# Optimization experiments

Measured on AMD Instinct MI355X. Metric: run time of the kernel, lower is better.

Reference implementation:

```python
import jax, jax.numpy as jnp
import numpy as np

# Dimensions
T = 1024      # tokens
D = 1024      # d_model
DFF = 1024    # expert intermediate dim
R = 64        # tucker rank (r_in == r_out)
G = 8         # n_group
E = 32        # experts_per_group
NEXP = G * E  # 256 routed experts
K = 8         # top-k


def setup_inputs() -> dict:
    key = jax.random.key(0)
    ks = jax.random.split(key, 12)
    s = 0.02
    return {
        "x": jax.random.normal(ks[0], (T, D), jnp.float32),
        "Wg": jax.random.normal(ks[1], (D, NEXP), jnp.float32) * s,
        "uin_gate": jax.random.normal(ks[2], (G, D, R), jnp.float32) * s,
        "core_gate": jax.random.normal(ks[3], (G, E, R, R), jnp.float32) * s,
        "uout_gate": jax.random.normal(ks[4], (G, R, DFF), jnp.float32) * s,
        "uin_up": jax.random.normal(ks[5], (G, D, R), jnp.float32) * s,
        "core_up": jax.random.normal(ks[6], (G, E, R, R), jnp.float32) * s,
        "uout_up": jax.random.normal(ks[7], (G, R, DFF), jnp.float32) * s,
        "uin_down": jax.random.normal(ks[8], (G, DFF, R), jnp.float32) * s,
        "core_down": jax.random.normal(ks[9], (G, E, R, R), jnp.float32) * s,
        "uout_down": jax.random.normal(ks[10], (G, R, D), jnp.float32) * s,
    }


def _moe_forward(x, Wg, uin_gate, core_gate, uout_gate,
                 uin_up, core_up, uout_up,
                 uin_down, core_down, uout_down):
    Tn, d = x.shape
    # Router: top-k over 256 experts, softmax over the k logits (fp32 as in torch)
    logits = x @ Wg                                   # [T, NEXP]
    w, sel = jax.lax.top_k(logits, K)                 # [T, K]
    w = jax.nn.softmax(w.astype(jnp.float32), axis=-1).astype(x.dtype)

    e = sel.reshape(-1)                               # [F] global expert id
    g = e // E                                        # [F] group id
    tok = jnp.repeat(jnp.arange(Tn), K)               # [F] source token id
    mask = (g[:, None] == jnp.arange(G)[None, :]).astype(x.dtype)  # [F, G]

    def gather_in(uin):
        # project tokens with every group's u_in once, then gather per pair
        pre = jnp.einsum('td,gdr->gtr', x, uin)       # [G, T, R]
        return pre[g, tok]                            # [F, R]

    def core_apply(xin, core):
        # per-pair Tucker core slice bmm: x.unsqueeze(1) @ core[rel_idx]
        slices = core.reshape(G * E, R, R)[e]         # [F, R, R] gather
        return jnp.einsum('fr,fro->fo', xin, slices)  # [F, R]

    def group_out(h, U):
        # per-pair group-specific projection: h[f] @ U[g_f]
        out = jnp.zeros((h.shape[0], U.shape[-1]), h.dtype)
        for gi in range(G):  # fixed small loop over 8 groups
            out = out + (h * mask[:, gi:gi + 1]) @ U[gi]
        return out

    gate_h = group_out(core_apply(gather_in(uin_gate), core_gate), uout_gate)  # [F, DFF]
    up_h = group_out(core_apply(gather_in(uin_up), core_up), uout_up)          # [F, DFF]
    act = jax.nn.silu(gate_h) * up_h                                           # SwiGLU
    xin_d = group_out(act, uin_down)                                           # [F, R]
    out_f = group_out(core_apply(xin_d, core_down), uout_down)                 # [F, D]
    out_f = out_f * w.reshape(-1)[:, None]
    # scatter-add expert outputs back to tokens
    return jax.ops.segment_sum(out_f, tok, num_segments=Tn)


def reference(x, Wg, uin_gate, core_gate, uout_gate,
              uin_up, core_up, uout_up,
              uin_down, core_down, uout_down):
    return _moe_forward(x, Wg, uin_gate, core_gate, uout_gate,
                        uin_up, core_up, uout_up,
                        uin_down, core_down, uout_down)
```

## Files before the change

### kernel.cpp

```cpp
#include <hip/hip_runtime.h>
#include <hip/hip_bf16.h>
#include <math.h>


#define T_ 1024
#define D_ 1024
#define DFF_ 1024
#define R_ 64
#define G_ 8
#define E_ 32
#define NEXP_ 256
#define K_ 8
#define F_ 8192
#define LKZ_ 8
#define LTB_ 8
#define PKZ_ 2
#define DKZ_ 4
#define LP_ 72

typedef short bf16x8 __attribute__((ext_vector_type(8)));
typedef float f32x4 __attribute__((ext_vector_type(4)));

__device__ __forceinline__ unsigned short f2bf(float f) {
  unsigned int u = __float_as_uint(f);
  u += 0x7fffu + ((u >> 16) & 1u);
  return (unsigned short)(u >> 16);
}

__device__ __forceinline__ void stage_tile(short* dst, const unsigned short* src,
                                           int gp, int tid) {
  for (int idx = tid; idx < 512; idx += 256) {
    int r = idx >> 3, c8 = (idx & 7) << 3;
    *(uint4*)&dst[r * LP_ + c8] = *(const uint4*)&src[(size_t)r * gp + c8];
  }
}

__device__ __forceinline__ void stage_tile_guard(short* dst, const unsigned short* src,
                                                 int gp, int rows_valid, int tid) {
  for (int idx = tid; idx < 512; idx += 256) {
    int r = idx >> 3, c8 = (idx & 7) << 3;
    uint4 v = make_uint4(0u, 0u, 0u, 0u);
    if (r < rows_valid) v = *(const uint4*)&src[(size_t)r * gp + c8];
    *(uint4*)&dst[r * LP_ + c8] = v;
  }
}

__device__ __forceinline__ void mma_strip(const short* As, const short* Bs,
                                          int ms, int lane, f32x4* acc) {
  int lm = lane & 15;
  int lk = (lane >> 4) << 3;
#pragma unroll
  for (int kc = 0; kc < 64; kc += 32) {
    bf16x8 a = *(const bf16x8*)&As[(ms + lm) * LP_ + kc + lk];
#pragma unroll
    for (int nt = 0; nt < 4; ++nt) {
      bf16x8 b = *(const bf16x8*)&Bs[(nt * 16 + lm) * LP_ + kc + lk];
      acc[nt] = __builtin_amdgcn_mfma_f32_16x16x32_bf16(a, b, acc[nt], 0, 0, 0);
    }
  }
}

__global__ __launch_bounds__(256) void k_prep_logits(
    const float* __restrict__ x, const float* __restrict__ Wg,
    const float* __restrict__ s0, const float* __restrict__ s1,
    const float* __restrict__ s2, const float* __restrict__ s3,
    const float* __restrict__ s4, const float* __restrict__ s5,
    unsigned short* __restrict__ xb,
    unsigned short* __restrict__ d0, unsigned short* __restrict__ d1,
    unsigned short* __restrict__ d2, unsigned short* __restrict__ d3,
    unsigned short* __restrict__ d4, unsigned short* __restrict__ d5,
    int* __restrict__ cnt, float* __restrict__ lp) {
  __shared__ float shbuf[64 * 65];
  int b = blockIdx.x;
  if (b < 896) {
    int id = b >> 7, rem = b & 127, g = rem >> 4, tile = rem & 15;
    if (id == 6) {
      size_t base = ((size_t)g * 16 + tile) * 8192;
      for (int i = threadIdx.x; i < 2048; i += 256) {
        size_t idx = base + (size_t)i * 4;
        float4 v = *(const float4*)&x[idx];
        xb[idx + 0] = f2bf(v.x);
        xb[idx + 1] = f2bf(v.y);
        xb[idx + 2] = f2bf(v.z);
        xb[idx + 3] = f2bf(v.w);
      }
      if (g == 0 && tile == 0) cnt[threadIdx.x] = 0;
      return;
    }
    const float* src = id == 0 ? s0 : id == 1 ? s1 : id == 2 ? s2 : id == 3 ? s3 : id == 4 ? s4 : s5;
    unsigned short* dst = id == 0 ? d0 : id == 1 ? d1 : id == 2 ? d2 : id == 3 ? d3 : id == 4 ? d4 : d5;
    if (id < 3) {
      int r0 = tile * 64;
      for (int idx = threadIdx.x; idx < 4096; idx += 256) {
        int r = idx >> 6, c = idx & 63;
        shbuf[r * 65 + c] = src[((size_t)g * 1024 + r0 + r) * 64 + c];
      }
      __syncthreads();
      for (int idx = threadIdx.x; idx < 4096; idx += 256) {
        int c = idx >> 6, r = idx & 63;
        dst[((size_t)g * 64 + c) * 1024 + r0 + r] = f2bf(shbuf[r * 65 + c]);
      }
    } else {
      int c0 = tile * 64;
      for (int idx = threadIdx.x; idx < 4096; idx += 256) {
        int r = idx >> 6, c = idx & 63;
        shbuf[r * 65 + c] = src[((size_t)g * 64 + r) * 1024 + c0 + c];
      }
      __syncthreads();
      if (id == 5) {
        for (int idx = threadIdx.x; idx < 4096; idx += 256) {
          int c = idx >> 6, r = idx & 63;
          dst[(size_t)(c0 + c) * 512 + g * 64 + r] = f2bf(shbuf[r * 65 + c]);
        }
      } else {
        for (int idx = threadIdx.x; idx < 4096; idx += 256) {
          int c = idx >> 6, r = idx & 63;
          dst[((size_t)g * 1024 + c0 + c) * 64 + r] = f2bf(shbuf[r * 65 + c]);
        }
      }
    }
    return;
  }
  int lb = b - 896;
  int t0 = (lb & 127) * LTB_;
  int z = lb >> 7;
  int e = threadIdx.x;
  float* xs = shbuf;
  float a[LTB_] = {};
  int dc = z * 128;
  {
    int idx = threadIdx.x * 4;
    int tl = idx >> 7, d = idx & 127;
    *(float4*)&xs[tl * 128 + d] = *(const float4*)&x[(size_t)(t0 + tl) * D_ + dc + d];
  }
  __syncthreads();
#pragma unroll 2
  for (int d2 = 0; d2 < 128; d2 += 4) {
    float w0 = Wg[(size_t)(dc + d2 + 0) * NEXP_ + e];
    float w1 = Wg[(size_t)(dc + d2 + 1) * NEXP_ + e];
    float w2 = Wg[(size_t)(dc + d2 + 2) * NEXP_ + e];
    float w3 = Wg[(size_t)(dc + d2 + 3) * NEXP_ + e];
#pragma unroll
    for (int j = 0; j < LTB_; ++j) {
      float4 xv = *(const float4*)&xs[j * 128 + d2];
      float aj = a[j];
      aj = fmaf(xv.x, w0, aj);
      aj = fmaf(xv.y, w1, aj);
      aj = fmaf(xv.z, w2, aj);
      aj = fmaf(xv.w, w3, aj);
      a[j] = aj;
    }
  }
  size_t base = (size_t)z * T_ * NEXP_;
#pragma unroll
  for (int j = 0; j < LTB_; ++j)
    lp[base + (size_t)(t0 + j) * NEXP_ + e] = a[j];
}

__global__ __launch_bounds__(256) void k_pre_topk(
    const unsigned short* __restrict__ xb,
    const unsigned short* __restrict__ uinT_g, const unsigned short* __restrict__ uinT_u,
    const float* __restrict__ lp,
    float* __restrict__ Pgp, float* __restrict__ Pup,
    int* __restrict__ sel, float* __restrict__ wsm,
    int* __restrict__ rank, int* __restrict__ cnt) {
  __shared__ short sh2[2 * 64 * LP_];
  int b = blockIdx.x;
  if (b < 512) {
    int tile = b & 15, g = (b >> 4) & 7, zz = b >> 7;
    int gu = zz >> 1, kz = zz & 1;
    const unsigned short* U = gu ? uinT_u : uinT_g;
    float* P = gu ? Pup : Pgp;
    int t0 = tile * 64;
    short* As = sh2;
    short* Bs = sh2 + 64 * LP_;
    int tid = threadIdx.x, lane = tid & 63, ms = (tid >> 6) * 16;
    f32x4 acc[4] = {};
    int dlo = kz * (D_ / PKZ_);
    for (int dc = dlo; dc < dlo + D_ / PKZ_; dc += 64) {
      stage_tile(As, xb + (size_t)t0 * D_ + dc, D_, tid);
      stage_tile(Bs, U + (size_t)g * 64 * 1024 + dc, 1024, tid);
      __syncthreads();
      mma_strip(As, Bs, ms, lane, acc);
      __syncthreads();
    }
    int lm = lane & 15, lq = (lane >> 4) * 4;
#pragma unroll
    for (int nt = 0; nt < 4; ++nt)
#pragma unroll
      for (int r = 0; r < 4; ++r)
        P[((size_t)(kz * G_ + g) * T_ + t0 + ms + lq + r) * R_ + nt * 16 + lm] = acc[nt][r];
    return;
  }
  int tb = b - 512;
  int wave = threadIdx.x >> 6;
  int lane = threadIdx.x & 63;
  int t = tb * 4 + wave;
  float v[4];
  int idx[4];
#pragma unroll
  for (int j = 0; j < 4; ++j) {
    idx[j] = lane + 64 * j;
    float s = 0.f;
#pragma unroll
    for (int z = 0; z < LKZ_; ++z)
      s += lp[(size_t)z * T_ * NEXP_ + (size_t)t * NEXP_ + idx[j]];
    v[j] = s;
  }
  float topv[K_];
  int topi[K_];
#pragma unroll
  for (int k = 0; k < K_; ++k) {
    float bv = v[0];
    int bi = idx[0];
#pragma unroll
    for (int j = 1; j < 4; ++j)
      if (v[j] > bv || (v[j] == bv && idx[j] < bi)) { bv = v[j]; bi = idx[j]; }
#pragma unroll
    for (int off = 32; off > 0; off >>= 1) {
      float ov = __shfl_xor(bv, off);
      int oi = __shfl_xor(bi, off);
      if (ov > bv || (ov == bv && oi < bi)) { bv = ov; bi = oi; }
    }
    topv[k] = bv;
    topi[k] = bi;
#pragma unroll
    for (int j = 0; j < 4; ++j)
      if (idx[j] == bi) v[j] = -INFINITY;
  }
  float m = topv[0];
  float ev[K_];
  float s = 0.f;
#pragma unroll
  for (int k = 0; k < K_; ++k) { ev[k] = expf(topv[k] - m); s += ev[k]; }
  float inv = 1.f / s;
  if (lane < K_) {
    sel[t * K_ + lane] = topi[lane];
    wsm[t * K_ + lane] = ev[lane] * inv;
    rank[t * K_ + lane] = atomicAdd(&cnt[topi[lane]], 1);
  }
}

__global__ __launch_bounds__(256) void k_scan(const int* __restrict__ cnt,
                                              int* __restrict__ off,
                                              const int* __restrict__ sel,
                                              const int* __restrict__ rank,
                                              int* __restrict__ ipos,
                                              int* __restrict__ pf) {
  __shared__ int s[NEXP_];
  __shared__ int ex[NEXP_];
  int i = threadIdx.x;
  int c0 = cnt[i];
  s[i] = c0;
  __syncthreads();
  for (int d = 1; d < NEXP_; d <<= 1) {
    int v = (i >= d) ? s[i - d] : 0;
    __syncthreads();
    s[i] += v;
    __syncthreads();
  }
  ex[i] = s[i] - c0;
  off[i + 1] = s[i];
  if (i == 0) off[0] = 0;
  __syncthreads();
#pragma unroll 4
  for (int f = i; f < F_; f += 256) {
    int p = ex[sel[f]] + rank[f];
    ipos[p] = f;
    pf[f] = p;
  }
}

__global__ __launch_bounds__(256) void k_core_gu(const float* __restrict__ Pgp,
                                                 const float* __restrict__ Pup,
                                                 const float* __restrict__ core_g,
                                                 const float* __restrict__ core_u,
                                                 const int* __restrict__ ipos,
                                                 const int* __restrict__ off,
                                                 unsigned short* __restrict__ xgb,
                                                 unsigned short* __restrict__ xub) {
  int e = blockIdx.x >> 1, half = blockIdx.x & 1;
  int g = e >> 5;
  __shared__ float cg[64 * 64], cu[64 * 64];
  __shared__ float rg[4][64], ru[4][64];
  int tid = threadIdx.x;
  for (int i = tid; i < 4096; i += 256) {
    cg[i] = core_g[(size_t)e * 4096 + i];
    cu[i] = core_u[(size_t)e * 4096 + i];
  }
  int p0 = off[e], n = off[e + 1] - p0;
  int hn = (n + 1) >> 1;
  int i0 = half * hn;
  int i1 = i0 + hn; if (i1 > n) i1 = n;
  int pl = tid >> 6, o = tid & 63;
  __syncthreads();
  for (int ib = i0; ib < i1; ib += 4) {
    int i = ib + pl;
    bool valid = i < i1;
    int p = p0 + i;
    float sg = 0.f, su = 0.f;
    if (valid) {
      int t = ipos[p] >> 3;
#pragma unroll
      for (int kz = 0; kz < PKZ_; ++kz) {
        sg += Pgp[((size_t)(kz * G_ + g) * T_ + t) * R_ + o];
        su += Pup[((size_t)(kz * G_ + g) * T_ + t) * R_ + o];
      }
    }
    __syncthreads();
    rg[pl][o] = sg;
    ru[pl][o] = su;
    __syncthreads();
    if (valid) {
      float ag = 0.f, au = 0.f;
#pragma unroll 8
      for (int r = 0; r < R_; ++r) {
        ag = fmaf(rg[pl][r], cg[r * R_ + o], ag);
        au = fmaf(ru[pl][r], cu[r * R_ + o], au);
      }
      xgb[(size_t)p * R_ + o] = f2bf(ag);
      xub[(size_t)p * R_ + o] = f2bf(au);
    }
  }
}

__global__ __launch_bounds__(256) void k_fused_ad(const unsigned short* __restrict__ xgb,
                                                  const unsigned short* __restrict__ xub,
                                                  const unsigned short* __restrict__ uoutT_g,
                                                  const unsigned short* __restrict__ uoutT_u,
                                                  const unsigned short* __restrict__ uinT_d,
                                                  const int* __restrict__ off,
                                                  float* __restrict__ xdp) {
  int g = blockIdx.y;
  int kz = blockIdx.z;
  int p0 = off[g * E_];
  int pend = off[g * E_ + E_];
  int ntiles = (pend - p0 + 63) >> 6;
  __shared__ short Ag[64 * LP_], Au[64 * LP_];
  __shared__ short Bg[64 * LP_], Bu[64 * LP_], Bd[64 * LP_];
  __shared__ short Pt[64 * LP_];
  int tid = threadIdx.x, lane = tid & 63, ms = (tid >> 6) * 16;
  int lm = lane & 15, lq = (lane >> 4) * 4;
  for (int tile = blockIdx.x; tile < ntiles; tile += gridDim.x) {
    int pbase = p0 + tile * 64;
    int rv = pend - pbase; if (rv > 64) rv = 64;
    stage_tile_guard(Ag, xgb + (size_t)pbase * R_, R_, rv, tid);
    stage_tile_guard(Au, xub + (size_t)pbase * R_, R_, rv, tid);
    f32x4 accd[4] = {};
#pragma unroll
    for (int c4 = 0; c4 < 4; ++c4) {
      int cc = kz * (DFF_ / DKZ_) + c4 * 64;
      stage_tile(Bg, uoutT_g + ((size_t)g * DFF_ + cc) * R_, R_, tid);
      stage_tile(Bu, uoutT_u + ((size_t)g * DFF_ + cc) * R_, R_, tid);
      stage_tile(Bd, uinT_d + (size_t)g * 64 * 1024 + cc, 1024, tid);
      __syncthreads();
      f32x4 accg[4] = {}, accu[4] = {};
      mma_strip(Ag, Bg, ms, lane, accg);
      mma_strip(Au, Bu, ms, lane, accu);
#pragma unroll
      for (int nt = 0; nt < 4; ++nt)
#pragma unroll
        for (int r = 0; r < 4; ++r) {
          float gv = accg[nt][r];
          float av = gv / (1.f + expf(-gv)) * accu[nt][r];
          Pt[(ms + lq + r) * LP_ + nt * 16 + lm] = (short)f2bf(av);
        }
      mma_strip(Pt, Bd, ms, lane, accd);
      __syncthreads();
    }
#pragma unroll
    for (int nt = 0; nt < 4; ++nt)
#pragma unroll
      for (int r = 0; r < 4; ++r) {
        int p = pbase + ms + lq + r;
        if (p < pend) xdp[((size_t)kz * F_ + p) * R_ + nt * 16 + lm] = accd[nt][r];
      }
    __syncthreads();
  }
}

__global__ __launch_bounds__(256) void k_down_core(const float* __restrict__ xdp,
                                                   const float* __restrict__ core_d,
                                                   const int* __restrict__ ipos,
                                                   const float* __restrict__ wsm,
                                                   const int* __restrict__ off,
                                                   float* __restrict__ zd) {
  int e = blockIdx.x >> 1, half = blockIdx.x & 1;
  __shared__ float cd[64 * 64];
  __shared__ float xs[4][64];
  int tid = threadIdx.x;
  for (int i = tid; i < 4096; i += 256) cd[i] = core_d[(size_t)e * 4096 + i];
  int p0 = off[e], n = off[e + 1] - p0;
  int hn = (n + 1) >> 1;
  int i0 = half * hn;
  int i1 = i0 + hn; if (i1 > n) i1 = n;
  int pl = tid >> 6, o = tid & 63;
  __syncthreads();
  for (int ib = i0; ib < i1; ib += 4) {
    int i = ib + pl;
    bool valid = i < i1;
    int p = p0 + i;
    float s = 0.f, w = 0.f;
    if (valid) {
#pragma unroll
      for (int kz = 0; kz < DKZ_; ++kz) s += xdp[((size_t)kz * F_ + p) * R_ + o];
      w = wsm[ipos[p]];
    }
    __syncthreads();
    xs[pl][o] = s;
    __syncthreads();
    if (valid) {
      float a = 0.f;
#pragma unroll 8
      for (int r = 0; r < R_; ++r) a = fmaf(xs[pl][r], cd[r * R_ + o], a);
      zd[(size_t)p * R_ + o] = w * a;
    }
  }
}

__global__ __launch_bounds__(256) void k_accY(const float* __restrict__ zd,
                                              const int* __restrict__ sel,
                                              const int* __restrict__ pf,
                                              unsigned short* __restrict__ Ybf) {
  int t = blockIdx.x * 4 + (threadIdx.x >> 6);
  int o = threadIdx.x & 63;
  float y[G_] = {};
#pragma unroll
  for (int k = 0; k < K_; ++k) {
    int f = t * K_ + k;
    int g = sel[f] >> 5;
    float v = zd[(size_t)pf[f] * R_ + o];
#pragma unroll
    for (int gi = 0; gi < G_; ++gi) y[gi] += (g == gi) ? v : 0.f;
  }
#pragma unroll
  for (int gi = 0; gi < G_; ++gi)
    Ybf[(size_t)t * 512 + gi * 64 + o] = f2bf(y[gi]);
}

__global__ __launch_bounds__(256) void k_fin(const unsigned short* __restrict__ Ybf,
                                             const unsigned short* __restrict__ Uod2T,
                                             float* __restrict__ out) {
  int t0 = blockIdx.x * 64;
  int d0 = blockIdx.y * 64;
  __shared__ short As[64 * LP_], Bs[64 * LP_];
  __shared__ float Os[64 * 68];
  int tid = threadIdx.x, lane = tid & 63, ms = (tid >> 6) * 16;
  int lm = lane & 15, lq = (lane >> 4) * 4;
  f32x4 acc[4] = {};
  for (int kc = 0; kc < 512; kc += 64) {
    stage_tile(As, Ybf + (size_t)t0 * 512 + kc, 512, tid);
    stage_tile(Bs, Uod2T + (size_t)d0 * 512 + kc, 512, tid);
    __syncthreads();
    mma_strip(As, Bs, ms, lane, acc);
    __syncthreads();
  }
#pragma unroll
  for (int nt = 0; nt < 4; ++nt)
#pragma unroll
    for (int r = 0; r < 4; ++r)
      Os[(ms + lq + r) * 68 + nt * 16 + lm] = acc[nt][r];
  __syncthreads();
  for (int idx = tid; idx < 1024; idx += 256) {
    int r = idx >> 4, c4 = (idx & 15) << 2;
    *(float4*)&out[(size_t)(t0 + r) * D_ + d0 + c4] = *(const float4*)&Os[r * 68 + c4];
  }
}

extern "C" void kernel_launch(void* const* d_in, const int* in_sizes, int n_in,
                              void* d_out, int out_size, void* d_ws, size_t ws_size,
                              hipStream_t stream) {
  const float* x = (const float*)d_in[0];
  const float* Wg = (const float*)d_in[1];
  const float* uin_gate = (const float*)d_in[2];
  const float* core_gate = (const float*)d_in[3];
  const float* uout_gate = (const float*)d_in[4];
  const float* uin_up = (const float*)d_in[5];
  const float* core_up = (const float*)d_in[6];
  const float* uout_up = (const float*)d_in[7];
  const float* uin_down = (const float*)d_in[8];
  const float* core_down = (const float*)d_in[9];
  const float* uout_down = (const float*)d_in[10];
  float* out = (float*)d_out;

  char* ws = (char*)d_ws;
  size_t o = 0;
  auto alloc = [&](size_t bytes) { size_t r = o; o = (o + bytes + 255) & ~(size_t)255; return r; };
  size_t o_lp = alloc((size_t)LKZ_ * T_ * NEXP_ * 4);
  size_t o_sel = alloc(F_ * 4);
  size_t o_wsm = alloc(F_ * 4);
  size_t o_rank = alloc(F_ * 4);
  size_t o_ipos = alloc(F_ * 4);
  size_t o_pf = alloc(F_ * 4);
  size_t o_cnt = alloc(NEXP_ * 4);
  size_t o_off = alloc((NEXP_ + 1) * 4);
  size_t o_xb = alloc((size_t)T_ * D_ * 2);
  size_t o_uinT_g = alloc((size_t)G_ * 64 * 1024 * 2);
  size_t o_uinT_u = alloc((size_t)G_ * 64 * 1024 * 2);
  size_t o_uinT_d = alloc((size_t)G_ * 64 * 1024 * 2);
  size_t o_uoutT_g = alloc((size_t)G_ * 1024 * 64 * 2);
  size_t o_uoutT_u = alloc((size_t)G_ * 1024 * 64 * 2);
  size_t o_Uod2T = alloc((size_t)D_ * 512 * 2);
  size_t o_xgb = alloc((size_t)F_ * R_ * 2);
  size_t o_xub = alloc((size_t)F_ * R_ * 2);
  size_t o_Y = alloc((size_t)T_ * 512 * 2);
  size_t o_pgp = alloc((size_t)PKZ_ * G_ * T_ * R_ * 4);
  size_t o_pup = alloc((size_t)PKZ_ * G_ * T_ * R_ * 4);
  size_t o_xdp = alloc((size_t)DKZ_ * F_ * R_ * 4);
  size_t o_zd = alloc((size_t)F_ * R_ * 4);
  (void)ws_size;

  float* lp = (float*)(ws + o_lp);
  int* sel = (int*)(ws + o_sel);
  float* wsm = (float*)(ws + o_wsm);
  int* rank = (int*)(ws + o_rank);
  int* ipos = (int*)(ws + o_ipos);
  int* pf = (int*)(ws + o_pf);
  int* cnt = (int*)(ws + o_cnt);
  int* off = (int*)(ws + o_off);
  unsigned short* xb = (unsigned short*)(ws + o_xb);
  unsigned short* uinT_g = (unsigned short*)(ws + o_uinT_g);
  unsigned short* uinT_u = (unsigned short*)(ws + o_uinT_u);
  unsigned short* uinT_d = (unsigned short*)(ws + o_uinT_d);
  unsigned short* uoutT_g = (unsigned short*)(ws + o_uoutT_g);
  unsigned short* uoutT_u = (unsigned short*)(ws + o_uoutT_u);
  unsigned short* Uod2T = (unsigned short*)(ws + o_Uod2T);
  unsigned short* xgb = (unsigned short*)(ws + o_xgb);
  unsigned short* xub = (unsigned short*)(ws + o_xub);
  unsigned short* Ybf = (unsigned short*)(ws + o_Y);
  float* pgp = (float*)(ws + o_pgp);
  float* pup = (float*)(ws + o_pup);
  float* xdp = (float*)(ws + o_xdp);
  float* zd = (float*)(ws + o_zd);

  k_prep_logits<<<1920, 256, 0, stream>>>(x, Wg, uin_gate, uin_up, uin_down,
                                          uout_gate, uout_up, uout_down, xb,
                                          uinT_g, uinT_u, uinT_d,
                                          uoutT_g, uoutT_u, Uod2T, cnt, lp);
  k_pre_topk<<<768, 256, 0, stream>>>(xb, uinT_g, uinT_u, lp, pgp, pup, sel, wsm, rank, cnt);
  k_scan<<<1, 256, 0, stream>>>(cnt, off, sel, rank, ipos, pf);
  k_core_gu<<<NEXP_ * 2, 256, 0, stream>>>(pgp, pup, core_gate, core_up, ipos, off, xgb, xub);
  k_fused_ad<<<dim3(16, G_, DKZ_), 256, 0, stream>>>(xgb, xub, uoutT_g, uoutT_u, uinT_d, off, xdp);
  k_down_core<<<NEXP_ * 2, 256, 0, stream>>>(xdp, core_down, ipos, wsm, off, zd);
  k_accY<<<T_ / 4, 256, 0, stream>>>(zd, sel, pf, Ybf);
  k_fin<<<dim3(16, 16), 256, 0, stream>>>(Ybf, Uod2T, out);
}
```

Baseline: 212.2 us.

## Replace scan scatter and accY with per-expert buckets and atomic Y accumulation

Top-k now writes pair ids straight into fixed-capacity per-expert bucket arrays, which removes the scan's scatter loop and the sel/rank/ipos/pf arrays. The down-core kernel atomically adds weighted results into an fp32 Y buffer that the prep kernel zero-fills. This drops the separate k_accY launch, and k_fin now converts fp32 Y to bf16 while staging. The router logits split also goes from 8 to 4 K-slices. The costs are atomic contention, nondeterministic float summation order, a larger bucket allocation, and twice the Y traffic in fp32.

```diff
diff --git a/kernel.cpp b/kernel.cpp
--- a/kernel.cpp
+++ b/kernel.cpp
@@ -12,7 +12,7 @@
 #define NEXP_ 256
 #define K_ 8
 #define F_ 8192
-#define LKZ_ 8
+#define LKZ_ 4
 #define LTB_ 8
 #define PKZ_ 2
 #define DKZ_ 4
@@ -42,6 +42,22 @@
     uint4 v = make_uint4(0u, 0u, 0u, 0u);
     if (r < rows_valid) v = *(const uint4*)&src[(size_t)r * gp + c8];
     *(uint4*)&dst[r * LP_ + c8] = v;
+  }
+}
+
+__device__ __forceinline__ void stage_tile_f32(short* dst, const float* src,
+                                               int gp, int tid) {
+  for (int idx = tid; idx < 512; idx += 256) {
+    int r = idx >> 3, c8 = (idx & 7) << 3;
+    const float* s = &src[(size_t)r * gp + c8];
+    float4 v0 = *(const float4*)s;
+    float4 v1 = *(const float4*)(s + 4);
+    uint4 u;
+    u.x = ((unsigned)f2bf(v0.y) << 16) | f2bf(v0.x);
+    u.y = ((unsigned)f2bf(v0.w) << 16) | f2bf(v0.z);
+    u.z = ((unsigned)f2bf(v1.y) << 16) | f2bf(v1.x);
+    u.w = ((unsigned)f2bf(v1.w) << 16) | f2bf(v1.z);
+    *(uint4*)&dst[r * LP_ + c8] = u;
   }
 }
 
@@ -69,7 +85,7 @@
     unsigned short* __restrict__ d0, unsigned short* __restrict__ d1,
     unsigned short* __restrict__ d2, unsigned short* __restrict__ d3,
     unsigned short* __restrict__ d4, unsigned short* __restrict__ d5,
-    int* __restrict__ cnt, float* __restrict__ lp) {
+    int* __restrict__ cnt, float* __restrict__ Yf, float* __restrict__ lp) {
   __shared__ float shbuf[64 * 65];
   int b = blockIdx.x;
   if (b < 896) {
@@ -84,6 +100,10 @@
         xb[idx + 2] = f2bf(v.z);
         xb[idx + 3] = f2bf(v.w);
       }
+      size_t ybase = ((size_t)g * 16 + tile) * 4096;
+      float4 z4 = make_float4(0.f, 0.f, 0.f, 0.f);
+      for (int i = threadIdx.x; i < 1024; i += 256)
+        *(float4*)&Yf[ybase + (size_t)i * 4] = z4;
       if (g == 0 && tile == 0) cnt[threadIdx.x] = 0;
       return;
     }
@@ -127,22 +147,23 @@
   int e = threadIdx.x;
   float* xs = shbuf;
   float a[LTB_] = {};
-  int dc = z * 128;
+  int dc = z * 256;
   {
-    int idx = threadIdx.x * 4;
-    int tl = idx >> 7, d = idx & 127;
-    *(float4*)&xs[tl * 128 + d] = *(const float4*)&x[(size_t)(t0 + tl) * D_ + dc + d];
+    int idx = threadIdx.x * 8;
+    int tl = idx >> 8, d = idx & 255;
+    *(float4*)&xs[tl * 256 + d] = *(const float4*)&x[(size_t)(t0 + tl) * D_ + dc + d];
+    *(float4*)&xs[tl * 256 + d + 4] = *(const float4*)&x[(size_t)(t0 + tl) * D_ + dc + d + 4];
   }
   __syncthreads();
 #pragma unroll 2
-  for (int d2 = 0; d2 < 128; d2 += 4) {
+  for (int d2 = 0; d2 < 256; d2 += 4) {
     float w0 = Wg[(size_t)(dc + d2 + 0) * NEXP_ + e];
     float w1 = Wg[(size_t)(dc + d2 + 1) * NEXP_ + e];
     float w2 = Wg[(size_t)(dc + d2 + 2) * NEXP_ + e];
     float w3 = Wg[(size_t)(dc + d2 + 3) * NEXP_ + e];
 #pragma unroll
     for (int j = 0; j < LTB_; ++j) {
-      float4 xv = *(const float4*)&xs[j * 128 + d2];
+      float4 xv = *(const float4*)&xs[j * 256 + d2];
       float aj = a[j];
       aj = fmaf(xv.x, w0, aj);
       aj = fmaf(xv.y, w1, aj);
@@ -162,8 +183,7 @@
     const unsigned short* __restrict__ uinT_g, const unsigned short* __restrict__ uinT_u,
     const float* __restrict__ lp,
     float* __restrict__ Pgp, float* __restrict__ Pup,
-    int* __restrict__ sel, float* __restrict__ wsm,
-    int* __restrict__ rank, int* __restrict__ cnt) {
+    float* __restrict__ wsm, int* __restrict__ bucket, int* __restrict__ cnt) {
   __shared__ short sh2[2 * 64 * LP_];
   int b = blockIdx.x;
   if (b < 512) {
@@ -235,23 +255,17 @@
   for (int k = 0; k < K_; ++k) { ev[k] = expf(topv[k] - m); s += ev[k]; }
   float inv = 1.f / s;
   if (lane < K_) {
-    sel[t * K_ + lane] = topi[lane];
     wsm[t * K_ + lane] = ev[lane] * inv;
-    rank[t * K_ + lane] = atomicAdd(&cnt[topi[lane]], 1);
+    int r1 = atomicAdd(&cnt[topi[lane]], 1);
+    bucket[topi[lane] * 1024 + r1] = t * K_ + lane;
   }
 }
 
 __global__ __launch_bounds__(256) void k_scan(const int* __restrict__ cnt,
-                                              int* __restrict__ off,
-                                              const int* __restrict__ sel,
-                                              const int* __restrict__ rank,
-                                              int* __restrict__ ipos,
-                                              int* __restrict__ pf) {
+                                              int* __restrict__ off) {
   __shared__ int s[NEXP_];
-  __shared__ int ex[NEXP_];
   int i = threadIdx.x;
-  int c0 = cnt[i];
-  s[i] = c0;
+  s[i] = cnt[i];
   __syncthreads();
   for (int d = 1; d < NEXP_; d <<= 1) {
     int v = (i >= d) ? s[i - d] : 0;
@@ -259,34 +273,26 @@
     s[i] += v;
     __syncthreads();
   }
-  ex[i] = s[i] - c0;
   off[i + 1] = s[i];
   if (i == 0) off[0] = 0;
-  __syncthreads();
-#pragma unroll 4
-  for (int f = i; f < F_; f += 256) {
-    int p = ex[sel[f]] + rank[f];
-    ipos[p] = f;
-    pf[f] = p;
-  }
 }
 
 __global__ __launch_bounds__(256) void k_core_gu(const float* __restrict__ Pgp,
                                                  const float* __restrict__ Pup,
                                                  const float* __restrict__ core_g,
                                                  const float* __restrict__ core_u,
-                                                 const int* __restrict__ ipos,
+                                                 const int* __restrict__ bucket,
                                                  const int* __restrict__ off,
                                                  unsigned short* __restrict__ xgb,
                                                  unsigned short* __restrict__ xub) {
   int e = blockIdx.x >> 1, half = blockIdx.x & 1;
   int g = e >> 5;
-  __shared__ float cg[64 * 64], cu[64 * 64];
+  __shared__ float cg[4096], cu[4096];
   __shared__ float rg[4][64], ru[4][64];
   int tid = threadIdx.x;
-  for (int i = tid; i < 4096; i += 256) {
-    cg[i] = core_g[(size_t)e * 4096 + i];
-    cu[i] = core_u[(size_t)e * 4096 + i];
+  for (int i = tid; i < 1024; i += 256) {
+    *(float4*)&cg[i * 4] = *(const float4*)&core_g[(size_t)e * 4096 + (size_t)i * 4];
+    *(float4*)&cu[i * 4] = *(const float4*)&core_u[(size_t)e * 4096 + (size_t)i * 4];
   }
   int p0 = off[e], n = off[e + 1] - p0;
   int hn = (n + 1) >> 1;
@@ -300,7 +306,7 @@
     int p = p0 + i;
     float sg = 0.f, su = 0.f;
     if (valid) {
-      int t = ipos[p] >> 3;
+      int t = bucket[e * 1024 + i] >> 3;
 #pragma unroll
       for (int kz = 0; kz < PKZ_; ++kz) {
         sg += Pgp[((size_t)(kz * G_ + g) * T_ + t) * R_ + o];
@@ -381,15 +387,17 @@
 
 __global__ __launch_bounds__(256) void k_down_core(const float* __restrict__ xdp,
                                                    const float* __restrict__ core_d,
-                                                   const int* __restrict__ ipos,
+                                                   const int* __restrict__ bucket,
                                                    const float* __restrict__ wsm,
                                                    const int* __restrict__ off,
-                                                   float* __restrict__ zd) {
+                                                   float* __restrict__ Yf) {
   int e = blockIdx.x >> 1, half = blockIdx.x & 1;
-  __shared__ float cd[64 * 64];
+  int g = e >> 5;
+  __shared__ float cd[4096];
   __shared__ float xs[4][64];
   int tid = threadIdx.x;
-  for (int i = tid; i < 4096; i += 256) cd[i] = core_d[(size_t)e * 4096 + i];
+  for (int i = tid; i < 1024; i += 256)
+    *(float4*)&cd[i * 4] = *(const float4*)&core_d[(size_t)e * 4096 + (size_t)i * 4];
   int p0 = off[e], n = off[e + 1] - p0;
   int hn = (n + 1) >> 1;
   int i0 = half * hn;
@@ -400,11 +408,11 @@
     int i = ib + pl;
     bool valid = i < i1;
     int p = p0 + i;
-    float s = 0.f, w = 0.f;
+    int f = valid ? bucket[e * 1024 + i] : 0;
+    float s = 0.f;
     if (valid) {
 #pragma unroll
       for (int kz = 0; kz < DKZ_; ++kz) s += xdp[((size_t)kz * F_ + p) * R_ + o];
-      w = wsm[ipos[p]];
     }
     __syncthreads();
     xs[pl][o] = s;
@@ -413,32 +421,12 @@
       float a = 0.f;
 #pragma unroll 8
       for (int r = 0; r < R_; ++r) a = fmaf(xs[pl][r], cd[r * R_ + o], a);
-      zd[(size_t)p * R_ + o] = w * a;
-    }
-  }
-}
-
-__global__ __launch_bounds__(256) void k_accY(const float* __restrict__ zd,
-                                              const int* __restrict__ sel,
-                                              const int* __restrict__ pf,
-                                              unsigned short* __restrict__ Ybf) {
-  int t = blockIdx.x * 4 + (threadIdx.x >> 6);
-  int o = threadIdx.x & 63;
-  float y[G_] = {};
-#pragma unroll
-  for (int k = 0; k < K_; ++k) {
-    int f = t * K_ + k;
-    int g = sel[f] >> 5;
-    float v = zd[(size_t)pf[f] * R_ + o];
-#pragma unroll
-    for (int gi = 0; gi < G_; ++gi) y[gi] += (g == gi) ? v : 0.f;
-  }
-#pragma unroll
-  for (int gi = 0; gi < G_; ++gi)
-    Ybf[(size_t)t * 512 + gi * 64 + o] = f2bf(y[gi]);
-}
-
-__global__ __launch_bounds__(256) void k_fin(const unsigned short* __restrict__ Ybf,
+      atomicAdd(&Yf[(size_t)(f >> 3) * 512 + g * 64 + o], wsm[f] * a);
+    }
+  }
+}
+
+__global__ __launch_bounds__(256) void k_fin(const float* __restrict__ Yf,
                                              const unsigned short* __restrict__ Uod2T,
                                              float* __restrict__ out) {
   int t0 = blockIdx.x * 64;
@@ -449,7 +437,7 @@
   int lm = lane & 15, lq = (lane >> 4) * 4;
   f32x4 acc[4] = {};
   for (int kc = 0; kc < 512; kc += 64) {
-    stage_tile(As, Ybf + (size_t)t0 * 512 + kc, 512, tid);
+    stage_tile_f32(As, Yf + (size_t)t0 * 512 + kc, 512, tid);
     stage_tile(Bs, Uod2T + (size_t)d0 * 512 + kc, 512, tid);
     __syncthreads();
     mma_strip(As, Bs, ms, lane, acc);
@@ -487,11 +475,8 @@
   size_t o = 0;
   auto alloc = [&](size_t bytes) { size_t r = o; o = (o + bytes + 255) & ~(size_t)255; return r; };
   size_t o_lp = alloc((size_t)LKZ_ * T_ * NEXP_ * 4);
-  size_t o_sel = alloc(F_ * 4);
   size_t o_wsm = alloc(F_ * 4);
-  size_t o_rank = alloc(F_ * 4);
-  size_t o_ipos = alloc(F_ * 4);
-  size_t o_pf = alloc(F_ * 4);
+  size_t o_bucket = alloc((size_t)NEXP_ * 1024 * 4);
   size_t o_cnt = alloc(NEXP_ * 4);
   size_t o_off = alloc((NEXP_ + 1) * 4);
   size_t o_xb = alloc((size_t)T_ * D_ * 2);
@@ -503,19 +488,15 @@
   size_t o_Uod2T = alloc((size_t)D_ * 512 * 2);
   size_t o_xgb = alloc((size_t)F_ * R_ * 2);
   size_t o_xub = alloc((size_t)F_ * R_ * 2);
-  size_t o_Y = alloc((size_t)T_ * 512 * 2);
+  size_t o_Y = alloc((size_t)T_ * 512 * 4);
   size_t o_pgp = alloc((size_t)PKZ_ * G_ * T_ * R_ * 4);
   size_t o_pup = alloc((size_t)PKZ_ * G_ * T_ * R_ * 4);
   size_t o_xdp = alloc((size_t)DKZ_ * F_ * R_ * 4);
-  size_t o_zd = alloc((size_t)F_ * R_ * 4);
   (void)ws_size;
 
   float* lp = (float*)(ws + o_lp);
-  int* sel = (int*)(ws + o_sel);
   float* wsm = (float*)(ws + o_wsm);
-  int* rank = (int*)(ws + o_rank);
-  int* ipos = (int*)(ws + o_ipos);
-  int* pf = (int*)(ws + o_pf);
+  int* bucket = (int*)(ws + o_bucket);
   int* cnt = (int*)(ws + o_cnt);
   int* off = (int*)(ws + o_off);
   unsigned short* xb = (unsigned short*)(ws + o_xb);
@@ -527,21 +508,19 @@
   unsigned short* Uod2T = (unsigned short*)(ws + o_Uod2T);
   unsigned short* xgb = (unsigned short*)(ws + o_xgb);
   unsigned short* xub = (unsigned short*)(ws + o_xub);
-  unsigned short* Ybf = (unsigned short*)(ws + o_Y);
+  float* Yf = (float*)(ws + o_Y);
   float* pgp = (float*)(ws + o_pgp);
   float* pup = (float*)(ws + o_pup);
   float* xdp = (float*)(ws + o_xdp);
-  float* zd = (float*)(ws + o_zd);
-
-  k_prep_logits<<<1920, 256, 0, stream>>>(x, Wg, uin_gate, uin_up, uin_down,
+
+  k_prep_logits<<<1408, 256, 0, stream>>>(x, Wg, uin_gate, uin_up, uin_down,
                                           uout_gate, uout_up, uout_down, xb,
                                           uinT_g, uinT_u, uinT_d,
-                                          uoutT_g, uoutT_u, Uod2T, cnt, lp);
-  k_pre_topk<<<768, 256, 0, stream>>>(xb, uinT_g, uinT_u, lp, pgp, pup, sel, wsm, rank, cnt);
-  k_scan<<<1, 256, 0, stream>>>(cnt, off, sel, rank, ipos, pf);
-  k_core_gu<<<NEXP_ * 2, 256, 0, stream>>>(pgp, pup, core_gate, core_up, ipos, off, xgb, xub);
+                                          uoutT_g, uoutT_u, Uod2T, cnt, Yf, lp);
+  k_pre_topk<<<768, 256, 0, stream>>>(xb, uinT_g, uinT_u, lp, pgp, pup, wsm, bucket, cnt);
+  k_scan<<<1, 256, 0, stream>>>(cnt, off);
+  k_core_gu<<<NEXP_ * 2, 256, 0, stream>>>(pgp, pup, core_gate, core_up, bucket, off, xgb, xub);
   k_fused_ad<<<dim3(16, G_, DKZ_), 256, 0, stream>>>(xgb, xub, uoutT_g, uoutT_u, uinT_d, off, xdp);
-  k_down_core<<<NEXP_ * 2, 256, 0, stream>>>(xdp, core_down, ipos, wsm, off, zd);
-  k_accY<<<T_ / 4, 256, 0, stream>>>(zd, sel, pf, Ybf);
-  k_fin<<<dim3(16, 16), 256, 0, stream>>>(Ybf, Uod2T, out);
-}
+  k_down_core<<<NEXP_ * 2, 256, 0, stream>>>(xdp, core_down, bucket, wsm, off, Yf);
+  k_fin<<<dim3(16, 16), 256, 0, stream>>>(Yf, Uod2T, out);
+}
```

After: 208.5 us. No clear change (-1.7%).
